# Optimization experiments

Hardware: AMD Instinct MI355X
Metric: run time of the kernel (lower is better)

## Reference

```python
import jax, jax.numpy as jnp
import numpy as np

F4_E2M1_MAX = 6.0
F8E4M3_MAX = 448.0
E4M3_EPS = 0.015625  # torch.finfo(float8_e4m3fn).tiny = 2**-6
BLOCK = 16
KE2M1 = jnp.array([0.0, 0.5, 1.0, 1.5, 2.0, 3.0, 4.0, 6.0], dtype=jnp.float32)


def round_to_e4m3(x):
    # emulate cast to float8_e4m3fn and back (round-to-nearest-even)
    return x.astype(jnp.float8_e4m3fn).astype(jnp.float32)


def fp4_121_positive(x):
    step1 = jnp.round(2.0 * x) / 2.0   # subnormal-ish region [0,2): step 0.5
    step2 = jnp.round(x)               # [2,4): step 1
    step3 = 2.0 * jnp.round(x / 2.0)   # [4,6]: step 2
    return jnp.where(x < 2.0, step1, jnp.where(x < 4.0, step2, step3))


def cast_to_fp4(x):
    return jnp.sign(x) * fp4_121_positive(jnp.abs(x))


def unpack_fp4_from_uint8(a, m, n):
    # a: int-typed tensor holding byte values in [0,256); two fp4 codes per byte
    high = (a.reshape(-1) >> 4) & 0xF
    low = a.reshape(-1) & 0xF
    combined = jnp.stack((low, high), axis=1).reshape(m, n)  # interleave low,high
    signs = (combined & 8) != 0
    abs_idx = combined & 7
    return KE2M1[abs_idx] * jnp.where(signs, -1.0, 1.0)


def dequant_nvfp4_packed(data_lp, out_scales, per_tensor_scale):
    m, half_n = data_lp.shape
    n = half_n * 2
    data_hp = unpack_fp4_from_uint8(data_lp, m, n)           # [m, n] float32
    scale_fp = out_scales / per_tensor_scale                  # [m, n/16]
    data_hp = data_hp.reshape(m, -1, BLOCK) * scale_fp.reshape(m, -1, 1)
    return data_hp.reshape(m, n)


def qdq_nvfp4(x):
    m, n = x.shape
    tensor_amax = jnp.max(jnp.abs(x))
    pts = jnp.clip(tensor_amax / F8E4M3_MAX, E4M3_EPS, F8E4M3_MAX)  # per-tensor scale
    xb = x.reshape(m, -1, BLOCK)
    block_scale = jnp.max(jnp.abs(xb), axis=-1) / F4_E2M1_MAX       # [m, n/16]
    scaled_bs = round_to_e4m3(jnp.clip(block_scale / pts, E4M3_EPS, F8E4M3_MAX))
    total_scale = pts * scaled_bs                                   # [m, n/16]
    data_scaled = jnp.clip(xb / total_scale[..., None], -F4_E2M1_MAX, F4_E2M1_MAX)
    data_lp = cast_to_fp4(data_scaled)                              # unpacked fp4 values
    # dequant: out_scales / (1/pts) == scaled_bs * pts == total_scale
    return (data_lp * total_scale[..., None]).reshape(m, n)


def setup_inputs() -> dict:
    key = jax.random.key(0)
    k1, k2, k3 = jax.random.split(key, 3)
    M, K, N = 16384, 2048, 2048  # tokens, in_features, out_features
    x = jax.random.normal(k1, (M, K), dtype=jnp.float32)
    weight_packed = jax.random.randint(k2, (N, K // 2), 0, 256, dtype=jnp.int32)
    # fp8-representable positive block scales
    weight_scale = round_to_e4m3(jax.random.uniform(k3, (N, K // 16), dtype=jnp.float32,
                                                    minval=0.05, maxval=1.0))
    weight_global_scale = jnp.ones((1,), dtype=jnp.float32)
    return {"x": x, "weight_packed": weight_packed,
            "weight_scale": weight_scale, "weight_global_scale": weight_global_scale}


def reference(x, weight_packed, weight_scale, weight_global_scale):
    hp_weight = dequant_nvfp4_packed(weight_packed, weight_scale, weight_global_scale)
    x_dq = qdq_nvfp4(x)
    return x_dq @ hp_weight.T
```

## Files before the change

kernel.cpp:

```cpp
#include <hip/hip_runtime.h>

typedef unsigned short u16;
typedef unsigned int u32;
typedef __attribute__((ext_vector_type(8))) short short8;
typedef __attribute__((ext_vector_type(4))) float floatx4;

static constexpr int M = 16384, N = 2048, K = 2048;


__device__ inline u16 f32_to_bf16(float x) {
    u32 u = __float_as_uint(x);
    u += 0x7FFFu + ((u >> 16) & 1u);
    return (u16)(u >> 16);
}

__device__ inline float e4m3_rne(float x) {
    u32 u = __float_as_uint(x);
    u += 0x7FFFFu + ((u >> 20) & 1u);
    u &= 0xFFF00000u;
    return __uint_as_float(u);
}

__device__ inline float fp4_dec(u32 c) {
    u32 e = (c >> 1) & 3u;
    float m = (float)(c & 1u);
    float v = e ? (2.0f + m) * (float)(1u << e) * 0.25f : 0.5f * m;
    return (c & 8u) ? -v : v;
}

__device__ inline float fp4_round_mag(float a) {
    if (a < 2.0f) return rintf(2.0f * a) * 0.5f;
    if (a < 4.0f) return rintf(a);
    return 2.0f * rintf(a * 0.5f);
}

__device__ inline float pts_from_amax(float amax) {
    return fminf(fmaxf(amax / 448.0f, 0.015625f), 448.0f);
}


__global__ __launch_bounds__(256) void amax_part(
    const float4* __restrict__ x, float* __restrict__ part,
    const int* __restrict__ wp, const float* __restrict__ wsc,
    const float* __restrict__ wgs, u16* __restrict__ wq) {
    int idx = blockIdx.x * blockDim.x + threadIdx.x;
    float m = 0.0f;
#pragma unroll 4
    for (int it = 0; it < 16; ++it) {
        float4 v = x[idx + it * 524288];
        m = fmaxf(m, fmaxf(fmaxf(fabsf(v.x), fabsf(v.y)),
                           fmaxf(fabsf(v.z), fabsf(v.w))));
    }

    float ginv = wgs[0];
#pragma unroll
    for (int g = 0; g < 4; g++) {
        int i = idx + g * 524288;
        int n = i >> 10;
        int kb = i & 1023;
        u32 byte = (u32)wp[i] & 0xFFu;
        float scale = wsc[(size_t)n * (K / 16) + (kb >> 3)] / ginv;
        float lo = fp4_dec(byte & 0xFu) * scale;
        float hi = fp4_dec((byte >> 4) & 0xFu) * scale;
        ((u32*)wq)[i] = (u32)f32_to_bf16(lo) | ((u32)f32_to_bf16(hi) << 16);
    }

#pragma unroll
    for (int off = 32; off > 0; off >>= 1)
        m = fmaxf(m, __shfl_down(m, off));
    __shared__ float sm[4];
    if ((threadIdx.x & 63) == 0) sm[threadIdx.x >> 6] = m;
    __syncthreads();
    if (threadIdx.x == 0)
        part[blockIdx.x] = fmaxf(fmaxf(sm[0], sm[1]), fmaxf(sm[2], sm[3]));
}


__global__ void amax_fin(const float* __restrict__ part, u32* __restrict__ out) {
    int t = threadIdx.x;
    float m = fmaxf(part[t], part[t + 1024]);
#pragma unroll
    for (int off = 32; off > 0; off >>= 1)
        m = fmaxf(m, __shfl_down(m, off));
    __shared__ float sm[16];
    if ((t & 63) == 0) sm[t >> 6] = m;
    __syncthreads();
    if (t < 16) {
        m = sm[t];
#pragma unroll
        for (int off = 8; off > 0; off >>= 1)
            m = fmaxf(m, __shfl_down(m, off));
        if (t == 0) *out = __float_as_uint(m);
    }
}


__global__ __launch_bounds__(256) void prep(
    const float4* __restrict__ x, uint2* __restrict__ aq,
    const u32* __restrict__ amax_bits) {
    int idx0 = blockIdx.x * blockDim.x + threadIdx.x;
    float pts = pts_from_amax(__uint_as_float(*amax_bits));

#pragma unroll 4
    for (int it = 0; it < 16; ++it) {
        int idx = idx0 + it * 524288;
        float4 v = x[idx];

        float bm = fmaxf(fmaxf(fabsf(v.x), fabsf(v.y)),
                         fmaxf(fabsf(v.z), fabsf(v.w)));
        bm = fmaxf(bm, __shfl_xor(bm, 1));
        bm = fmaxf(bm, __shfl_xor(bm, 2));

        float bs = bm / 6.0f;
        float sbs = e4m3_rne(fminf(fmaxf(bs / pts, 0.015625f), 448.0f));
        float ts = pts * sbs;

        float vf[4] = {v.x, v.y, v.z, v.w};
        u16 o[4];
#pragma unroll
        for (int i = 0; i < 4; i++) {
            float s = vf[i] / ts;
            s = fminf(fmaxf(s, -6.0f), 6.0f);
            float lp = copysignf(fp4_round_mag(fabsf(s)), s);
            o[i] = f32_to_bf16(lp * sbs);
        }
        aq[idx] = *(const uint2*)o;
    }
}


#define GLDS(g, l)                                                              \
    __builtin_amdgcn_global_load_lds(                                           \
        (const __attribute__((address_space(1))) unsigned int*)(g),             \
        (__attribute__((address_space(3))) unsigned int*)(l), 16, 0, 0)

__global__ __launch_bounds__(512, 2) void gemm_bt(
    const u16* __restrict__ A, const u16* __restrict__ B,
    float* __restrict__ C, const u32* __restrict__ amax_bits)
{
    __shared__ u16 sh[2][2][2][8192];

    const int tid = threadIdx.x;
    const int w = tid >> 6, lane = tid & 63;

    const int id = blockIdx.x;
    const int xcd = id & 7;
    const int local = id >> 3;
    const int bm = xcd * 8 + (local >> 3);
    const int bn = local & 7;

    const int wm = w >> 2, wn = w & 3;
    const int r16 = lane & 15, q = lane >> 4;

    floatx4 acc[8][4] = {};

    const int swz = (r16 & 7) << 4;
    const int aoff0 = r16 * 64 + (((q * 16) ^ swz) >> 1);
    const int aoff1 = r16 * 64 + (((64 + q * 16) ^ swz) >> 1);

    const int srow8 = lane >> 3;
    const int scol = ((lane & 7) ^ srow8) * 8;
    const u16* gA[2], * gB[2];
    gA[0] = A + (size_t)(bm * 256 + (w * 2 + 0) * 8 + srow8) * K + scol;
    gA[1] = A + (size_t)(bm * 256 + (w * 2 + 1) * 8 + srow8) * K + scol;
    gB[0] = B + (size_t)(bn * 256 + (w * 2 + 0) * 8 + srow8) * K + scol;
    gB[1] = B + (size_t)(bn * 256 + (w * 2 + 1) * 8 + srow8) * K + scol;

#define STG(buf, mat, half, ktc) do {                                           \
        const u16* _s0 = ((mat) ? gB[0] : gA[0]) + (size_t)(half) * 128 * K + (ktc); \
        const u16* _s1 = ((mat) ? gB[1] : gA[1]) + (size_t)(half) * 128 * K + (ktc); \
        GLDS(_s0, &sh[buf][mat][half][w * 1024]);                               \
        GLDS(_s1, &sh[buf][mat][half][w * 1024 + 512]);                         \
    } while (0)

    short8 aF[4][2], bF[4][2];

#define RD_A(buf, Qa) do {                                                      \
        const u16* _ar = &sh[buf][0][wm][(Qa) * 4096];                          \
        _Pragma("unroll") for (int _i = 0; _i < 4; _i++) {                      \
            aF[_i][0] = *(const short8*)(_ar + _i * 1024 + aoff0);              \
            aF[_i][1] = *(const short8*)(_ar + _i * 1024 + aoff1); }            \
    } while (0)

#define RD_B(buf, Qb) do {                                                      \
        const u16* _br = &sh[buf][1][wn >> 1][(wn & 1) * 4096 + (Qb) * 2048];   \
        _Pragma("unroll") for (int _j = 0; _j < 2; _j++) {                      \
            bF[(Qb) * 2 + _j][0] = *(const short8*)(_br + _j * 1024 + aoff0);   \
            bF[(Qb) * 2 + _j][1] = *(const short8*)(_br + _j * 1024 + aoff1); } \
    } while (0)

#define MMAQ(Qa, Qb)                                                            \
        _Pragma("unroll") for (int _i = 0; _i < 4; _i++)                        \
        _Pragma("unroll") for (int _j = 0; _j < 2; _j++)                        \
        _Pragma("unroll") for (int _k = 0; _k < 2; _k++)                        \
            acc[(Qa) * 4 + _i][(Qb) * 2 + _j] =                                 \
                __builtin_amdgcn_mfma_f32_16x16x32_bf16(                        \
                    aF[_i][_k], bF[(Qb) * 2 + _j][_k],                          \
                    acc[(Qa) * 4 + _i][(Qb) * 2 + _j], 0, 0, 0)

#define BAR do { __builtin_amdgcn_sched_barrier(0);                             \
                 __builtin_amdgcn_s_barrier();                                  \
                 __builtin_amdgcn_sched_barrier(0); } while (0)
#define PRIO1 __builtin_amdgcn_s_setprio(1)
#define PRIO0 do { __builtin_amdgcn_s_setprio(0);                               \
                   __builtin_amdgcn_sched_barrier(0); } while (0)
#define ENDPH do { __builtin_amdgcn_s_barrier();                                \
                   __builtin_amdgcn_sched_barrier(0); } while (0)
#define CHK4 do { asm volatile("s_waitcnt vmcnt(4)" ::: "memory");              \
                  __builtin_amdgcn_sched_barrier(0); } while (0)

    STG(0, 0, 0, 0); STG(0, 0, 1, 0);
    STG(0, 1, 0, 0); STG(0, 1, 1, 0);
    STG(1, 1, 0, 64); STG(1, 1, 1, 64);
    CHK4;
    __builtin_amdgcn_s_barrier();

#pragma unroll 1
    for (int it = 0; it < K / 128; ++it) {
        const int ktY  = (2 * it + 1) * 64;
        const int kx2  = 2 * it + 2, ky2 = 2 * it + 3;
        const int ktX2 = (kx2 <= 31 ? kx2 : 31) * 64;
        const int ktY2 = (ky2 <= 31 ? ky2 : 31) * 64;

        RD_A(0, 0); RD_B(0, 0); STG(1, 0, 0, ktY);
        BAR; PRIO1; MMAQ(0, 0); PRIO0; ENDPH;
        RD_B(0, 1); STG(1, 0, 1, ktY);
        BAR; PRIO1; MMAQ(0, 1); PRIO0; ENDPH;
        RD_A(0, 1); STG(0, 1, 0, ktX2); STG(0, 1, 1, ktX2);
        BAR; PRIO1; MMAQ(1, 1); MMAQ(1, 0); PRIO0; CHK4; ENDPH;
        RD_A(1, 0); RD_B(1, 0); STG(0, 0, 0, ktX2);
        BAR; PRIO1; MMAQ(0, 0); PRIO0; ENDPH;
        RD_B(1, 1); STG(0, 0, 1, ktX2);
        BAR; PRIO1; MMAQ(0, 1); PRIO0; ENDPH;
        RD_A(1, 1); STG(1, 1, 0, ktY2); STG(1, 1, 1, ktY2);
        BAR; PRIO1; MMAQ(1, 1); MMAQ(1, 0); PRIO0; CHK4; ENDPH;
    }

    asm volatile("s_waitcnt vmcnt(0)" ::: "memory");
    __builtin_amdgcn_s_barrier();
    __builtin_amdgcn_sched_barrier(0);

    float pts = pts_from_amax(__uint_as_float(*amax_bits));

    float* stage = (float*)&sh[0][0][0][0] + w * 1024;
    const int erow = lane >> 4;
    const int ecol = lane & 15;
    float* Cb = C + (size_t)(bm * 256 + wm * 128) * N + bn * 256 + wn * 64;
#pragma unroll
    for (int i = 0; i < 8; i++) {
#pragma unroll
        for (int j = 0; j < 4; j++)
#pragma unroll
            for (int t = 0; t < 4; t++)
                stage[(q * 4 + t) * 64 + j * 16 + r16] = pts * acc[i][j][t];
        asm volatile("s_waitcnt lgkmcnt(0)" ::: "memory");
        __builtin_amdgcn_sched_barrier(0);
#pragma unroll
        for (int k4 = 0; k4 < 4; k4++) {
            float4 vv = *(const float4*)&stage[(k4 * 4 + erow) * 64 + ecol * 4];
            *(float4*)&Cb[(size_t)(i * 16 + k4 * 4 + erow) * N + ecol * 4] = vv;
        }
        asm volatile("s_waitcnt lgkmcnt(0)" ::: "memory");
        __builtin_amdgcn_sched_barrier(0);
    }
}


extern "C" void kernel_launch(void* const* d_in, const int* in_sizes, int n_in,
                              void* d_out, int out_size, void* d_ws, size_t ws_size,
                              hipStream_t stream) {
    const float* x   = (const float*)d_in[0];
    const int*   wp  = (const int*)d_in[1];
    const float* wsc = (const float*)d_in[2];
    const float* wgs = (const float*)d_in[3];
    float* out = (float*)d_out;

    u32*   amax_bits = (u32*)d_ws;
    float* part      = (float*)((char*)d_ws + 64);
    u16*   aq        = (u16*)((char*)d_ws + 16384);
    u16*   wq        = aq + (size_t)M * K;

    amax_part<<<2048, 256, 0, stream>>>((const float4*)x, part,
                                        wp, wsc, wgs, wq);
    amax_fin<<<1, 1024, 0, stream>>>(part, amax_bits);
    prep<<<2048, 256, 0, stream>>>((const float4*)x, (uint2*)aq, amax_bits);
    gemm_bt<<<512, 512, 0, stream>>>(aq, wq, out, amax_bits);
}
```

Before: 374.9 us.

## Reschedule GEMM main loop into 8 phases with double-buffered LDS fragment reads

Restructures the main loop from six phases with two barriers each into eight phases with one barrier each. Shared-memory reads for the next MFMA group are issued before the current group's barrier, into double-buffered A/B fragment registers, so reads overlap compute. Per-phase vmcnt waits are tuned to the new staging order. The epilogue staging buffer gets an XOR swizzle to reduce LDS bank conflicts. The extra fragment registers raise register pressure, and the finer waits risk stalls or ordering hazards.

```diff
diff --git a/kernel.cpp b/kernel.cpp
--- a/kernel.cpp
+++ b/kernel.cpp
@@ -173,47 +173,53 @@
         GLDS(_s1, &sh[buf][mat][half][w * 1024 + 512]);                         \
     } while (0)
 
-    short8 aF[4][2], bF[4][2];
-
-#define RD_A(buf, Qa) do {                                                      \
+    short8 aF[2][4][2];
+    short8 bF[2][2][2][2];
+
+#define RDA(buf, Qa, s) do {                                                    \
         const u16* _ar = &sh[buf][0][wm][(Qa) * 4096];                          \
         _Pragma("unroll") for (int _i = 0; _i < 4; _i++) {                      \
-            aF[_i][0] = *(const short8*)(_ar + _i * 1024 + aoff0);              \
-            aF[_i][1] = *(const short8*)(_ar + _i * 1024 + aoff1); }            \
+            aF[s][_i][0] = *(const short8*)(_ar + _i * 1024 + aoff0);           \
+            aF[s][_i][1] = *(const short8*)(_ar + _i * 1024 + aoff1); }         \
     } while (0)
 
-#define RD_B(buf, Qb) do {                                                      \
+#define RDB(buf, Qb) do {                                                       \
         const u16* _br = &sh[buf][1][wn >> 1][(wn & 1) * 4096 + (Qb) * 2048];   \
         _Pragma("unroll") for (int _j = 0; _j < 2; _j++) {                      \
-            bF[(Qb) * 2 + _j][0] = *(const short8*)(_br + _j * 1024 + aoff0);   \
-            bF[(Qb) * 2 + _j][1] = *(const short8*)(_br + _j * 1024 + aoff1); } \
+            bF[buf][Qb][_j][0] = *(const short8*)(_br + _j * 1024 + aoff0);     \
+            bF[buf][Qb][_j][1] = *(const short8*)(_br + _j * 1024 + aoff1); }   \
     } while (0)
 
-#define MMAQ(Qa, Qb)                                                            \
+#define MMAQ(s, buf, Qa, Qb)                                                    \
         _Pragma("unroll") for (int _i = 0; _i < 4; _i++)                        \
         _Pragma("unroll") for (int _j = 0; _j < 2; _j++)                        \
         _Pragma("unroll") for (int _k = 0; _k < 2; _k++)                        \
             acc[(Qa) * 4 + _i][(Qb) * 2 + _j] =                                 \
                 __builtin_amdgcn_mfma_f32_16x16x32_bf16(                        \
-                    aF[_i][_k], bF[(Qb) * 2 + _j][_k],                          \
+                    aF[s][_i][_k], bF[buf][Qb][_j][_k],                         \
                     acc[(Qa) * 4 + _i][(Qb) * 2 + _j], 0, 0, 0)
 
-#define BAR do { __builtin_amdgcn_sched_barrier(0);                             \
-                 __builtin_amdgcn_s_barrier();                                  \
-                 __builtin_amdgcn_sched_barrier(0); } while (0)
+#define VM6 do { asm volatile("s_waitcnt vmcnt(6)" ::: "memory"); } while (0)
+#define VM4 do { asm volatile("s_waitcnt vmcnt(4)" ::: "memory"); } while (0)
+#define BARX do { __builtin_amdgcn_sched_barrier(0);                            \
+                  __builtin_amdgcn_s_barrier();                                 \
+                  __builtin_amdgcn_sched_barrier(0); } while (0)
 #define PRIO1 __builtin_amdgcn_s_setprio(1)
 #define PRIO0 do { __builtin_amdgcn_s_setprio(0);                               \
                    __builtin_amdgcn_sched_barrier(0); } while (0)
-#define ENDPH do { __builtin_amdgcn_s_barrier();                                \
-                   __builtin_amdgcn_sched_barrier(0); } while (0)
-#define CHK4 do { asm volatile("s_waitcnt vmcnt(4)" ::: "memory");              \
-                  __builtin_amdgcn_sched_barrier(0); } while (0)
-
-    STG(0, 0, 0, 0); STG(0, 0, 1, 0);
-    STG(0, 1, 0, 0); STG(0, 1, 1, 0);
-    STG(1, 1, 0, 64); STG(1, 1, 1, 64);
-    CHK4;
+
+    STG(0, 1, 0, 0);
+    STG(0, 1, 1, 0);
+    STG(0, 0, 0, 0);
+    STG(0, 0, 1, 0);
+    STG(1, 1, 0, 64);
+    STG(1, 1, 1, 64);
+    STG(1, 0, 0, 64);
+    asm volatile("s_waitcnt vmcnt(6)" ::: "memory");
     __builtin_amdgcn_s_barrier();
+    __builtin_amdgcn_sched_barrier(0);
+    RDA(0, 0, 0);
+    RDB(0, 0);
 
 #pragma unroll 1
     for (int it = 0; it < K / 128; ++it) {
@@ -222,18 +228,14 @@
         const int ktX2 = (kx2 <= 31 ? kx2 : 31) * 64;
         const int ktY2 = (ky2 <= 31 ? ky2 : 31) * 64;
 
-        RD_A(0, 0); RD_B(0, 0); STG(1, 0, 0, ktY);
-        BAR; PRIO1; MMAQ(0, 0); PRIO0; ENDPH;
-        RD_B(0, 1); STG(1, 0, 1, ktY);
-        BAR; PRIO1; MMAQ(0, 1); PRIO0; ENDPH;
-        RD_A(0, 1); STG(0, 1, 0, ktX2); STG(0, 1, 1, ktX2);
-        BAR; PRIO1; MMAQ(1, 1); MMAQ(1, 0); PRIO0; CHK4; ENDPH;
-        RD_A(1, 0); RD_B(1, 0); STG(0, 0, 0, ktX2);
-        BAR; PRIO1; MMAQ(0, 0); PRIO0; ENDPH;
-        RD_B(1, 1); STG(0, 0, 1, ktX2);
-        BAR; PRIO1; MMAQ(0, 1); PRIO0; ENDPH;
-        RD_A(1, 1); STG(1, 1, 0, ktY2); STG(1, 1, 1, ktY2);
-        BAR; PRIO1; MMAQ(1, 1); MMAQ(1, 0); PRIO0; CHK4; ENDPH;
+        RDB(0, 1);    STG(1, 0, 1, ktY);  VM6; BARX; PRIO1; MMAQ(0, 0, 0, 0); PRIO0;
+        RDA(0, 1, 1); STG(0, 1, 0, ktX2); VM6; BARX; PRIO1; MMAQ(0, 0, 0, 1); PRIO0;
+        RDB(1, 0);    STG(0, 1, 1, ktX2); VM4; BARX; PRIO1; MMAQ(1, 0, 1, 1); PRIO0;
+        RDA(1, 0, 0); STG(0, 0, 0, ktX2); VM6; BARX; PRIO1; MMAQ(1, 0, 1, 0); PRIO0;
+        RDB(1, 1);    STG(0, 0, 1, ktX2); VM6; BARX; PRIO1; MMAQ(0, 1, 0, 0); PRIO0;
+        RDA(1, 1, 1); STG(1, 1, 0, ktY2); VM6; BARX; PRIO1; MMAQ(0, 1, 0, 1); PRIO0;
+        RDB(0, 0);    STG(1, 1, 1, ktY2); VM4; BARX; PRIO1; MMAQ(1, 1, 1, 1); PRIO0;
+        RDA(0, 0, 0); STG(1, 0, 0, ktY2); VM6; BARX; PRIO1; MMAQ(1, 1, 1, 0); PRIO0;
     }
 
     asm volatile("s_waitcnt vmcnt(0)" ::: "memory");
@@ -252,12 +254,14 @@
         for (int j = 0; j < 4; j++)
 #pragma unroll
             for (int t = 0; t < 4; t++)
-                stage[(q * 4 + t) * 64 + j * 16 + r16] = pts * acc[i][j][t];
+                stage[(q * 4 + t) * 64 + ((j * 16 + r16) ^ ((q & 1) << 4))] =
+                    pts * acc[i][j][t];
         asm volatile("s_waitcnt lgkmcnt(0)" ::: "memory");
         __builtin_amdgcn_sched_barrier(0);
 #pragma unroll
         for (int k4 = 0; k4 < 4; k4++) {
-            float4 vv = *(const float4*)&stage[(k4 * 4 + erow) * 64 + ecol * 4];
+            float4 vv = *(const float4*)&stage[(k4 * 4 + erow) * 64 +
+                                               ((ecol * 4) ^ ((k4 & 1) << 4))];
             *(float4*)&Cb[(size_t)(i * 16 + k4 * 4 + erow) * N + ecol * 4] = vv;
         }
         asm volatile("s_waitcnt lgkmcnt(0)" ::: "memory");
```

Result: slower. 490.6 us (+30.9%).
